# Kernel optimization log

Measured on AMD Instinct MI355X. Metric: run time of the kernel, lower is better.

The kernel has to match this reference:

```python
import jax, jax.numpy as jnp
import numpy as np
import math

B, T, D, H = 16, 256, 1024, 1024
SEG = 16              # segment_len
S = T // SEG          # number of cached segment slots (max_cached_segments=None)
SCALE = 1.0 / math.sqrt(H)


def _ln(x, g, b, eps=1e-5):
    m = jnp.mean(x, -1, keepdims=True)
    v = jnp.mean((x - m) ** 2, -1, keepdims=True)
    return (x - m) * jax.lax.rsqrt(v + eps) * g + b


def _lstm_cell(inp, h, c, Wih, Whh, bih, bhh):
    z = inp @ Wih.T + bih + h @ Whh.T + bhh
    i, f, g, o = jnp.split(z, 4, axis=-1)  # torch LSTMCell gate order i,f,g,o
    c2 = jax.nn.sigmoid(f) * c + jax.nn.sigmoid(i) * jnp.tanh(g)
    return jax.nn.sigmoid(o) * jnp.tanh(c2), c2


def setup_inputs() -> dict:
    key = jax.random.key(0)
    it = iter(jax.random.split(key, 40))

    def un(shape, fan):
        lim = 1.0 / np.sqrt(fan)
        return jax.random.uniform(next(it), shape, jnp.float32, -lim, lim)

    inp = {}
    inp['x'] = jax.random.normal(next(it), (B, T, D), jnp.float32)
    inp['W_ip'] = un((D, D), D); inp['b_ip'] = un((D,), D)
    inp['g_ip'] = jnp.ones((D,), jnp.float32); inp['be_ip'] = jnp.zeros((D,), jnp.float32)
    inp['W_ih0'] = un((4 * H, D), H); inp['W_hh0'] = un((4 * H, H), H)
    inp['b_ih0'] = un((4 * H,), H); inp['b_hh0'] = un((4 * H,), H)
    inp['W_ih1'] = un((4 * H, H), H); inp['W_hh1'] = un((4 * H, H), H)
    inp['b_ih1'] = un((4 * H,), H); inp['b_hh1'] = un((4 * H,), H)
    inp['Wq'] = un((H, H), H); inp['Wk'] = un((H, H), H); inp['Wv'] = un((H, H), H)
    inp['Wg1'] = un((H, 3 * H), 3 * H); inp['bg1'] = un((H,), 3 * H)
    inp['Wg2'] = un((H, H), H); inp['bg2'] = un((H,), H)
    inp['Wo'] = un((H, H), H); inp['bo'] = un((H,), H)
    inp['Wf'] = un((H, 2 * H), 2 * H); inp['bf'] = un((H,), 2 * H)
    inp['g_f'] = jnp.ones((H,), jnp.float32); inp['be_f'] = jnp.zeros((H,), jnp.float32)
    return inp


def reference(x, W_ip, b_ip, g_ip, be_ip,
              W_ih0, W_hh0, b_ih0, b_hh0,
              W_ih1, W_hh1, b_ih1, b_hh1,
              Wq, Wk, Wv, Wg1, bg1, Wg2, bg2, Wo, bo,
              Wf, bf, g_f, be_f):
    # input_proj (eval mode: dropout = identity)
    xp = jax.nn.relu(_ln(x @ W_ip.T + b_ip, g_ip, be_ip))      # [B,T,D]
    xseg = xp.transpose(1, 0, 2).reshape(S, SEG, B, D)          # [S,SEG,B,D]

    def seg_body(carry, xs):
        h0, c0, h1, c1, kbank, vbank = carry
        x_s, s = xs                                             # x_s:[SEG,B,D], s = #cached segments
        valid = jnp.arange(S) < s

        def step(inner, xt):
            h0, c0, h1, c1, seg_sum = inner
            h0, c0 = _lstm_cell(xt, h0, c0, W_ih0, W_hh0, b_ih0, b_hh0)
            h1, c1 = _lstm_cell(h0, h1, c1, W_ih1, W_hh1, b_ih1, b_hh1)
            # SegmentMemoryRetriever, cache_mode='gated_residual'
            q = h1 @ Wq.T
            scores = jnp.einsum('bh,sbh->bs', q, kbank) * SCALE
            scores = jnp.where(valid[None, :], scores, -1e9)
            attn = jax.nn.softmax(scores, axis=-1)
            retrieved = jnp.einsum('bs,sbh->bh', attn, vbank)
            gi = jnp.concatenate([h1, retrieved, h1 - retrieved], -1)
            gate = jax.nn.sigmoid(jax.nn.relu(gi @ Wg1.T + bg1) @ Wg2.T + bg2)
            out = (gate * h1 + (1.0 - gate) * retrieved) @ Wo.T + bo
            ret = jnp.where(s > 0, out, jnp.zeros_like(out))    # empty cache -> zero retrieval
            enh = jax.nn.relu(_ln(jnp.concatenate([h1, ret], -1) @ Wf.T + bf, g_f, be_f))
            return (h0, c0, h1, c1, seg_sum + h1), enh

        init = (h0, c0, h1, c1, jnp.zeros_like(h1))
        (h0, c0, h1, c1, seg_sum), enh = jax.lax.scan(step, init, x_s)
        # append segment to cache; keys/values projected once (linear, equivalent)
        kbank = kbank.at[s].set((seg_sum / SEG) @ Wk.T)         # context = segment mean (use_segment_context)
        vbank = vbank.at[s].set(h1 @ Wv.T)                      # memory = last top hidden of segment
        return (h0, c0, h1, c1, kbank, vbank), enh

    z = jnp.zeros((B, H), x.dtype)
    bank = jnp.zeros((S, B, H), x.dtype)
    carry0 = (z, z, z, z, bank, bank)
    _, enh = jax.lax.scan(seg_body, carry0, (xseg, jnp.arange(S)))
    return enh.reshape(T, B, H).transpose(1, 0, 2)              # sequence_output [B,T,H]
```

## Files before the change

kernel.cpp:

```cpp
#include <hip/hip_runtime.h>
#include <hip/hip_bf16.h>
#include <math.h>

#define B_ 16
#define T_ 256
#define D_ 1024
#define H_ 1024
#define S_ 16
#define SCALE_ (1.0f/32.0f)

typedef __attribute__((ext_vector_type(8))) short short8v;
typedef __attribute__((ext_vector_type(4))) float f32x4;

__device__ __forceinline__ float sigm(float x) { return 1.f / (1.f + expf(-x)); }

__device__ __forceinline__ ushort f2b(float v) {
  __hip_bfloat16 h = __float2bfloat16(v);
  return *reinterpret_cast<ushort*>(&h);
}
__device__ __forceinline__ float b2f(ushort u) {
  union { unsigned u32; float f; } x; x.u32 = ((unsigned)u) << 16; return x.f;
}

__device__ __forceinline__ void glds16(const void* g, void* l) {
  __builtin_amdgcn_global_load_lds((const __attribute__((address_space(1))) void*)g,
                                   (__attribute__((address_space(3))) void*)l, 16, 0, 0);
}

__device__ __forceinline__ void waitflags64(const int* f, int lane) {
  for (;;) {
    int v = __hip_atomic_load(f + lane, __ATOMIC_RELAXED, __HIP_MEMORY_SCOPE_AGENT);
    if (__all(v != 0)) return;
    __builtin_amdgcn_s_sleep(1);
  }
}

__device__ __forceinline__ void publish_pair(ushort* base, int tid, ushort hb) {
  unsigned hi = (unsigned)__shfl_down((int)hb, 1);
  if (!(tid & 1)) {
    unsigned word = (unsigned)hb | (hi << 16);
    __hip_atomic_exchange((unsigned*)base, word,
                          __ATOMIC_RELAXED, __HIP_MEMORY_SCOPE_AGENT);
  }
}

__device__ __forceinline__ float block_sum256(float v) {
  __shared__ float lds[4];
  #pragma unroll
  for (int off = 32; off; off >>= 1) v += __shfl_down(v, off);
  int w = threadIdx.x >> 6;
  if ((threadIdx.x & 63) == 0) lds[w] = v;
  __syncthreads();
  float r = lds[0] + lds[1] + lds[2] + lds[3];
  __syncthreads();
  return r;
}

#define NJOBS 14
struct CvtJobs {
  const float* src[NJOBS];
  ushort* dst[NJOBS];
  int cum[NJOBS + 1];
};

__global__ __launch_bounds__(256)
void cvt_all(CvtJobs J)
{
  int i = blockIdx.x * 256 + threadIdx.x;
  if (i >= J.cum[NJOBS]) return;
  int j = 0;
  #pragma unroll
  for (int k = 1; k < NJOBS; ++k) j += (i >= J.cum[k]) ? 1 : 0;
  int idx = i - J.cum[j];
  float4 v = ((const float4*)J.src[j])[idx];
  ushort4 o; o.x = f2b(v.x); o.y = f2b(v.y); o.z = f2b(v.z); o.w = f2b(v.w);
  ((ushort4*)J.dst[j])[idx] = o;
}

__global__ __launch_bounds__(256)
void cvt_bf16(const float* __restrict__ in, ushort* __restrict__ out, int n)
{
  int i = (blockIdx.x * 256 + threadIdx.x) * 4;
  if (i >= n) return;
  float4 v = *(const float4*)(in + i);
  ushort4 o; o.x = f2b(v.x); o.y = f2b(v.y); o.z = f2b(v.z); o.w = f2b(v.w);
  *(ushort4*)(out + i) = o;
}

template<int ACT, int REMAP>
__global__ __launch_bounds__(256)
void gemm_bf16(const ushort* __restrict__ A, const ushort* __restrict__ W,
               const float* __restrict__ bias,
               float* __restrict__ Cf, ushort* __restrict__ Cb,
               int M, int N, int K, float ascale, int ldc,
               const ushort* __restrict__ Hx, const float* __restrict__ Rx)
{
  __shared__ char As[16384];
  __shared__ char Bs[16384];
  const int tid = threadIdx.x;
  const int w = tid >> 6, l = tid & 63;
  const int m0 = blockIdx.y * 128, n0 = blockIdx.x * 128;
  const int wm = w >> 1, wn = w & 1;
  const int srow = l >> 3;
  const int sbyte = ((l & 7) * 16) ^ (srow << 4);
  f32x4 acc[4][4];
  #pragma unroll
  for (int i = 0; i < 4; ++i)
    #pragma unroll
    for (int j = 0; j < 4; ++j) acc[i][j] = (f32x4){0.f, 0.f, 0.f, 0.f};

  for (int k0 = 0; k0 < K; k0 += 64) {
    __syncthreads();
    #pragma unroll
    for (int c = 0; c < 4; ++c) {
      int ca = w * 4 + c;
      int r = ca * 8 + srow;
      glds16((const char*)A + (((size_t)(m0 + r) * K + k0) << 1) + sbyte, As + ca * 1024);
      glds16((const char*)W + (((size_t)(n0 + r) * K + k0) << 1) + sbyte, Bs + ca * 1024);
    }
    __syncthreads();
    #pragma unroll
    for (int ks = 0; ks < 2; ++ks) {
      short8v a[4], b[4];
      int qb = ks * 64 + (l >> 4) * 16;
      #pragma unroll
      for (int i = 0; i < 4; ++i) {
        int ra = wm * 64 + i * 16 + (l & 15);
        a[i] = *(const short8v*)(As + ra * 128 + (qb ^ ((ra & 7) << 4)));
        int rb = wn * 64 + i * 16 + (l & 15);
        b[i] = *(const short8v*)(Bs + rb * 128 + (qb ^ ((rb & 7) << 4)));
      }
      #pragma unroll
      for (int i = 0; i < 4; ++i)
        #pragma unroll
        for (int j = 0; j < 4; ++j)
          acc[i][j] = __builtin_amdgcn_mfma_f32_16x16x32_bf16(a[i], b[j], acc[i][j], 0, 0, 0);
    }
  }
  #pragma unroll
  for (int i = 0; i < 4; ++i) {
    #pragma unroll
    for (int j = 0; j < 4; ++j) {
      int n = n0 + wn * 64 + j * 16 + (l & 15);
      float bv = bias ? bias[n] : 0.f;
      #pragma unroll
      for (int q = 0; q < 4; ++q) {
        int m = m0 + wm * 64 + i * 16 + (l >> 4) * 4 + q;
        float v = acc[i][j][q] * ascale + bv;
        if (ACT == 1) v = fmaxf(v, 0.f);
        if (ACT == 2) v = sigm(v);
        if (ACT == 3) {
          float gte = sigm(v);
          float h = b2f(Hx[(size_t)m * 1024 + n]);
          float r = Rx[(size_t)m * 1024 + n];
          v = gte * h + (1.f - gte) * r;
        }
        if (ACT == 4) v = (m >= 256) ? v : 0.f;
        size_t off = REMAP ? ((size_t)((m & 255) * 16 + (m >> 8)) * ldc + n)
                           : ((size_t)m * ldc + n);
        if (Cf) Cf[off] = v;
        if (Cb) Cb[off] = f2b(v);
      }
    }
  }
}

__global__ __launch_bounds__(256)
void ln_relu_bf16(const float* __restrict__ X, const float* __restrict__ g,
                  const float* __restrict__ be, ushort* __restrict__ out)
{
  size_t row = blockIdx.x;
  const float4* p = (const float4*)(X + row * 1024);
  int tid = threadIdx.x;
  float4 v = p[tid];
  float s = block_sum256(v.x + v.y + v.z + v.w);
  float mean = s * (1.f / 1024.f);
  float dx = v.x - mean, dy = v.y - mean, dz = v.z - mean, dw = v.w - mean;
  float ss = block_sum256(dx*dx + dy*dy + dz*dz + dw*dw);
  float r = rsqrtf(ss * (1.f / 1024.f) + 1e-5f);
  int c4 = tid * 4;
  ushort4 o;
  o.x = f2b(fmaxf(dx * r * g[c4+0] + be[c4+0], 0.f));
  o.y = f2b(fmaxf(dy * r * g[c4+1] + be[c4+1], 0.f));
  o.z = f2b(fmaxf(dz * r * g[c4+2] + be[c4+2], 0.f));
  o.w = f2b(fmaxf(dw * r * g[c4+3] + be[c4+3], 0.f));
  *(ushort4*)(out + row * 1024 + c4) = o;
}

__global__ __launch_bounds__(256)
void ln_relu_final(const float* __restrict__ F, const float* __restrict__ g,
                   const float* __restrict__ be, float* __restrict__ out)
{
  int row = blockIdx.x;
  int t = row >> 4, b = row & 15;
  const float4* p = (const float4*)(F + (size_t)row * 1024);
  int tid = threadIdx.x;
  float4 v = p[tid];
  float s = block_sum256(v.x + v.y + v.z + v.w);
  float mean = s * (1.f / 1024.f);
  float dx = v.x - mean, dy = v.y - mean, dz = v.z - mean, dw = v.w - mean;
  float ss = block_sum256(dx*dx + dy*dy + dz*dz + dw*dw);
  float r = rsqrtf(ss * (1.f / 1024.f) + 1e-5f);
  int c4 = tid * 4;
  float4 o;
  o.x = fmaxf(dx * r * g[c4+0] + be[c4+0], 0.f);
  o.y = fmaxf(dy * r * g[c4+1] + be[c4+1], 0.f);
  o.z = fmaxf(dz * r * g[c4+2] + be[c4+2], 0.f);
  o.w = fmaxf(dw * r * g[c4+3] + be[c4+3], 0.f);
  ((float4*)(out + ((size_t)b * T_ + t) * 1024))[tid] = o;
}

__global__ __launch_bounds__(512)
void lstm_persistent(const ushort* __restrict__ Z0T,
                     const ushort* __restrict__ whh0,
                     const float* __restrict__ bhh0,
                     const ushort* __restrict__ wih1,
                     const ushort* __restrict__ whh1,
                     const float* __restrict__ bih1,
                     const float* __restrict__ bhh1,
                     ushort* __restrict__ HP,
                     ushort* __restrict__ H1B,
                     const ushort* __restrict__ ZP,
                     float* __restrict__ KSUM,
                     int* flag0,
                     int* flag1)
{
  __shared__ char Ah[65536];
  __shared__ float zs[8][16][16];
  __builtin_amdgcn_fence(__ATOMIC_ACQUIRE, "agent");
  const int tid = threadIdx.x, w = tid >> 6, l = tid & 63;
  const int lm = l & 15, lq = l >> 4;
  const int g = w & 3, kh = w >> 2;
  const int jb = blockIdx.x & 63;
  const int j0 = jb * 16;
  const int eb = tid >> 4, ej = tid & 15, jf = j0 + ej;
  float creg = 0.f;
  float br[4];

  if (blockIdx.x < 64) {
    short8v wreg[16];
    {
      const int n = g * 1024 + j0 + lm;
      const ushort* wb = whh0 + (size_t)n * 1024 + kh * 512 + lq * 8;
      #pragma unroll
      for (int ks = 0; ks < 16; ++ks) wreg[ks] = *(const short8v*)(wb + ks * 32);
    }
    if (tid < 256) {
      #pragma unroll
      for (int gg = 0; gg < 4; ++gg) br[gg] = bhh0[gg * 1024 + jf];
    }
    for (int t = 0; t < T_; ++t) {
      float z0v[4];
      if (tid < 256) {
        const ushort* zp = Z0T + ((size_t)t * 16 + eb) * 4096 + jf;
        #pragma unroll
        for (int gg = 0; gg < 4; ++gg) z0v[gg] = b2f(zp[gg * 1024]);
      }
      if (t > 0) {
        if (w == 0) waitflags64(flag0 + (size_t)t * 64, l);
        __syncthreads();
      }
      const ushort* hin = HP + (size_t)t * 16384;
      #pragma unroll
      for (int it = 0; it < 4; ++it) {
        int g1k = w * 4 + it;
        int kc = g1k * 4 + lq;
        int m = lm ^ (kc & 15);
        glds16(hin + (size_t)m * 1024 + kc * 8, Ah + g1k * 1024);
      }
      __syncthreads();
      {
        f32x4 a0 = {0.f,0.f,0.f,0.f}, a1 = {0.f,0.f,0.f,0.f};
        #pragma unroll
        for (int ks = 0; ks < 16; ks += 2) {
          int kc0 = kh * 64 + ks * 4 + lq;
          int kc1 = kc0 + 4;
          short8v f0 = *(const short8v*)(Ah + kc0 * 256 + ((lm ^ (kc0 & 15)) << 4));
          short8v f1 = *(const short8v*)(Ah + kc1 * 256 + ((lm ^ (kc1 & 15)) << 4));
          a0 = __builtin_amdgcn_mfma_f32_16x16x32_bf16(f0, wreg[ks],     a0, 0, 0, 0);
          a1 = __builtin_amdgcn_mfma_f32_16x16x32_bf16(f1, wreg[ks + 1], a1, 0, 0, 0);
        }
        #pragma unroll
        for (int q = 0; q < 4; ++q) zs[w][lq * 4 + q][lm] = a0[q] + a1[q];
      }
      __syncthreads();
      if (tid < 256) {
        float zi = zs[0][eb][ej] + zs[4][eb][ej] + z0v[0] + br[0];
        float zf = zs[1][eb][ej] + zs[5][eb][ej] + z0v[1] + br[1];
        float zg = zs[2][eb][ej] + zs[6][eb][ej] + z0v[2] + br[2];
        float zo = zs[3][eb][ej] + zs[7][eb][ej] + z0v[3] + br[3];
        float cp = sigm(zf) * creg + sigm(zi) * tanhf(zg);
        creg = cp;
        ushort hb = f2b(sigm(zo) * tanhf(cp));
        publish_pair(HP + (size_t)(t + 1) * 16384 + eb * 1024 + jf, tid, hb);
      }
      __syncthreads();
      if (tid == 0)
        __hip_atomic_store(flag0 + (size_t)(t + 1) * 64 + jb, 1,
                           __ATOMIC_RELAXED, __HIP_MEMORY_SCOPE_AGENT);
    }
  } else {
    short8v wreg[32];
    {
      const int n = g * 1024 + j0 + lm;
      const ushort* wb = (kh ? whh1 : wih1) + (size_t)n * 1024 + lq * 8;
      #pragma unroll
      for (int ks = 0; ks < 32; ++ks) wreg[ks] = *(const short8v*)(wb + ks * 32);
    }
    if (tid < 256) {
      #pragma unroll
      for (int gg = 0; gg < 4; ++gg)
        br[gg] = bih1[gg * 1024 + jf] + bhh1[gg * 1024 + jf];
    }
    float ksr = 0.f;
    for (int t = 0; t < T_; ++t) {
      if (w == 0) waitflags64(flag0 + (size_t)(t + 1) * 64, l);
      __syncthreads();
      const ushort* h0n = HP + (size_t)(t + 1) * 16384;
      #pragma unroll
      for (int it = 0; it < 4; ++it) {
        int g1k = w * 4 + it;
        int kc = g1k * 4 + lq;
        int m = lm ^ (kc & 15);
        glds16(h0n + (size_t)m * 1024 + kc * 8, Ah + g1k * 1024);
      }
      if (w == 1 && t > 0) waitflags64(flag1 + (size_t)(t - 1) * 64, l);
      __syncthreads();
      const ushort* h1p = (t > 0) ? (H1B + (size_t)(t - 1) * 16384) : ZP;
      #pragma unroll
      for (int it = 0; it < 4; ++it) {
        int g1k = 32 + w * 4 + it;
        int kc = g1k * 4 + lq;
        int m = lm ^ (kc & 15);
        glds16(h1p + (size_t)m * 1024 + (kc - 128) * 8, Ah + g1k * 1024);
      }
      __syncthreads();
      {
        f32x4 a0 = {0.f,0.f,0.f,0.f}, a1 = {0.f,0.f,0.f,0.f};
        #pragma unroll
        for (int ks = 0; ks < 32; ks += 2) {
          int kc0 = kh * 128 + ks * 4 + lq;
          int kc1 = kc0 + 4;
          short8v f0 = *(const short8v*)(Ah + kc0 * 256 + ((lm ^ (kc0 & 15)) << 4));
          short8v f1 = *(const short8v*)(Ah + kc1 * 256 + ((lm ^ (kc1 & 15)) << 4));
          a0 = __builtin_amdgcn_mfma_f32_16x16x32_bf16(f0, wreg[ks],     a0, 0, 0, 0);
          a1 = __builtin_amdgcn_mfma_f32_16x16x32_bf16(f1, wreg[ks + 1], a1, 0, 0, 0);
        }
        #pragma unroll
        for (int q = 0; q < 4; ++q) zs[w][lq * 4 + q][lm] = a0[q] + a1[q];
      }
      __syncthreads();
      if (tid < 256) {
        float zi = zs[0][eb][ej] + zs[4][eb][ej] + br[0];
        float zf = zs[1][eb][ej] + zs[5][eb][ej] + br[1];
        float zg = zs[2][eb][ej] + zs[6][eb][ej] + br[2];
        float zo = zs[3][eb][ej] + zs[7][eb][ej] + br[3];
        float cp = sigm(zf) * creg + sigm(zi) * tanhf(zg);
        creg = cp;
        float hv = sigm(zo) * tanhf(cp);
        ksr += hv;
        publish_pair(H1B + (size_t)t * 16384 + eb * 1024 + jf, tid, f2b(hv));
        if ((t & 15) == 15) {
          KSUM[((size_t)(t >> 4) * 16 + eb) * 1024 + jf] = ksr;
          ksr = 0.f;
        }
      }
      __syncthreads();
      if (tid == 0)
        __hip_atomic_store(flag1 + (size_t)t * 64 + jb, 1,
                           __ATOMIC_RELAXED, __HIP_MEMORY_SCOPE_AGENT);
    }
  }
}

__global__ __launch_bounds__(256)
void vgather(const ushort* __restrict__ H1B, ushort* __restrict__ VINB)
{
  int i = blockIdx.x * 256 + threadIdx.x;
  int row = i >> 8, c4 = (i & 255) * 4;
  int src = (row >> 4) * 256 + 240 + (row & 15);
  *(ushort4*)(VINB + (size_t)row * 1024 + c4) =
      *(const ushort4*)(H1B + (size_t)src * 1024 + c4);
}

__global__ __launch_bounds__(256)
void attn_kernel(const float* __restrict__ Q, const float* __restrict__ kbank,
                 const float* __restrict__ vbank, float* __restrict__ R)
{
  int row = blockIdx.x;
  int t = row >> 4, b = row & 15;
  int si = t >> 4;
  int tid = threadIdx.x, lane = tid & 63, w = tid >> 6;
  if (si == 0) {
    float4 z = {0.f, 0.f, 0.f, 0.f};
    ((float4*)(R + (size_t)row * 1024))[tid] = z;
    return;
  }
  __shared__ float sc[16];
  const float* q = Q + (size_t)row * 1024;
  for (int s = w; s < si; s += 4) {
    const float* kk = kbank + ((size_t)s * 16 + b) * 1024;
    float p = 0.f;
    for (int k = lane; k < 1024; k += 64) p += q[k] * kk[k];
    #pragma unroll
    for (int off = 32; off; off >>= 1) p += __shfl_down(p, off);
    if (lane == 0) sc[s] = p * SCALE_;
  }
  __syncthreads();
  float mx = -1e30f;
  for (int s = 0; s < si; ++s) mx = fmaxf(mx, sc[s]);
  float den = 0.f;
  for (int s = 0; s < si; ++s) den += expf(sc[s] - mx);
  float inv = 1.f / den;
  float4 accv = {0.f, 0.f, 0.f, 0.f};
  for (int s = 0; s < si; ++s) {
    float a = expf(sc[s] - mx) * inv;
    float4 vv = ((const float4*)(vbank + ((size_t)s * 16 + b) * 1024))[tid];
    accv.x += a * vv.x; accv.y += a * vv.y; accv.z += a * vv.z; accv.w += a * vv.w;
  }
  ((float4*)(R + (size_t)row * 1024))[tid] = accv;
}

__global__ __launch_bounds__(256)
void build_gi_cat(const ushort* __restrict__ H1B, const float* __restrict__ R,
                  ushort* __restrict__ GI, ushort* __restrict__ CATB)
{
  size_t r = blockIdx.x;
  int c4 = threadIdx.x * 4;
  ushort4 h4 = *(const ushort4*)(H1B + r * 1024 + c4);
  float4 rv = *(const float4*)(R + r * 1024 + c4);
  *(ushort4*)(GI + r * 3072 + c4) = h4;
  ushort4 rb; rb.x = f2b(rv.x); rb.y = f2b(rv.y); rb.z = f2b(rv.z); rb.w = f2b(rv.w);
  *(ushort4*)(GI + r * 3072 + 1024 + c4) = rb;
  ushort4 d;
  d.x = f2b(b2f(h4.x) - rv.x); d.y = f2b(b2f(h4.y) - rv.y);
  d.z = f2b(b2f(h4.z) - rv.z); d.w = f2b(b2f(h4.w) - rv.w);
  *(ushort4*)(GI + r * 3072 + 2048 + c4) = d;
  *(ushort4*)(CATB + r * 2048 + c4) = h4;
}

extern "C" void kernel_launch(void* const* d_in, const int* in_sizes, int n_in,
                              void* d_out, int out_size, void* d_ws, size_t ws_size,
                              hipStream_t stream) {
  const float* x     = (const float*)d_in[0];
  const float* W_ip  = (const float*)d_in[1];
  const float* b_ip  = (const float*)d_in[2];
  const float* g_ip  = (const float*)d_in[3];
  const float* be_ip = (const float*)d_in[4];
  const float* W_ih0 = (const float*)d_in[5];
  const float* W_hh0 = (const float*)d_in[6];
  const float* b_ih0 = (const float*)d_in[7];
  const float* b_hh0 = (const float*)d_in[8];
  const float* W_ih1 = (const float*)d_in[9];
  const float* W_hh1 = (const float*)d_in[10];
  const float* b_ih1 = (const float*)d_in[11];
  const float* b_hh1 = (const float*)d_in[12];
  const float* Wq    = (const float*)d_in[13];
  const float* Wk    = (const float*)d_in[14];
  const float* Wv    = (const float*)d_in[15];
  const float* Wg1   = (const float*)d_in[16];
  const float* bg1   = (const float*)d_in[17];
  const float* Wg2   = (const float*)d_in[18];
  const float* bg2   = (const float*)d_in[19];
  const float* Wo    = (const float*)d_in[20];
  const float* bo    = (const float*)d_in[21];
  const float* Wf    = (const float*)d_in[22];
  const float* bff   = (const float*)d_in[23];
  const float* g_f   = (const float*)d_in[24];
  const float* be_f  = (const float*)d_in[25];
  float* out = (float*)d_out;
  char* ws = (char*)d_ws;
  const size_t MB = (size_t)1 << 20;
  const size_t KB = (size_t)1 << 10;

  ushort* WB = (ushort*)(ws);
  ushort* wipB  = WB;
  ushort* wih0B = WB + 1*1048576;
  ushort* whh0B = WB + 5*1048576;
  ushort* wih1B = WB + 9*1048576;
  ushort* whh1B = WB + 13*1048576;
  ushort* wqB   = WB + 17*1048576;
  ushort* wkB   = WB + 18*1048576;
  ushort* wvB   = WB + 19*1048576;
  ushort* wg1B  = WB + 20*1048576;
  ushort* wg2B  = WB + 23*1048576;
  ushort* woB   = WB + 24*1048576;
  ushort* wfB   = WB + 25*1048576;

  ushort* XB   = (ushort*)(ws + 54 * MB);
  float*  XP   = (float*)(ws + 62 * MB);
  float*  Qf   = XP;
  char*   SCR  = ws + 78 * MB;
  ushort* Z0T  = (ushort*)SCR;
  ushort* GIB  = (ushort*)SCR;
  ushort* CATB = (ushort*)(SCR + 24 * MB);
  ushort* G1B  = (ushort*)(SCR + 40 * MB);
  ushort* MIXB = (ushort*)SCR;
  float*  FB   = (float*)SCR;
  ushort* H1B  = (ushort*)(ws + 126 * MB);
  ushort* HP   = (ushort*)(ws + 134 * MB);
  float*  R    = (float*)(ws + 134 * MB);
  char*   ST   = ws + 150 * MB;
  int*    flag0 = (int*)(ST);
  int*    flag1 = (int*)(ST + 68 * KB);
  const ushort* ZPc = (const ushort*)(ST + 132 * KB);
  float*  KSUM = (float*)(ST + 192 * KB);
  ushort* KSB  = (ushort*)(ST + 1216 * KB);
  float*  KBf  = (float*)(ST + 1728 * KB);
  float*  VBf  = (float*)(ST + 2752 * KB);
  ushort* VINB = (ushort*)(ST + 3776 * KB);

  hipMemsetAsync(ST, 0, 164 * KB, stream);
  hipMemsetAsync(HP, 0, 32 * KB, stream);

  dim3 blk(256);
  {
    CvtJobs J;
    const float* srcs[NJOBS] = { x, W_ip, W_ih0, W_hh0, W_ih1, W_hh1,
                                 Wq, Wk, Wv, Wg1, Wg2, Wo, Wf, nullptr };
    ushort* dsts[NJOBS] = { XB, wipB, wih0B, whh0B, wih1B, whh1B,
                            wqB, wkB, wvB, wg1B, wg2B, woB, wfB, nullptr };
    int n4[NJOBS] = { 1048576, 262144, 1048576, 1048576, 1048576, 1048576,
                      262144, 262144, 262144, 786432, 262144, 262144,
                      524288, 0 };
    int c = 0;
    for (int j = 0; j < NJOBS; ++j) {
      J.src[j] = srcs[j] ? srcs[j] : x;
      J.dst[j] = dsts[j] ? dsts[j] : XB;
      J.cum[j] = c;
      c += n4[j];
    }
    J.cum[NJOBS] = c;
    cvt_all<<<dim3((c + 255) / 256), blk, 0, stream>>>(J);
  }

  gemm_bf16<0,0><<<dim3(1024/128, 4096/128), blk, 0, stream>>>(
      XB, wipB, b_ip, XP, nullptr, 4096, 1024, 1024, 1.f, 1024, nullptr, nullptr);
  ln_relu_bf16<<<4096, blk, 0, stream>>>(XP, g_ip, be_ip, XB);
  gemm_bf16<0,1><<<dim3(4096/128, 4096/128), blk, 0, stream>>>(
      XB, wih0B, b_ih0, nullptr, Z0T, 4096, 4096, 1024, 1.f, 4096, nullptr, nullptr);
  {
    void* kargs[] = {
      (void*)&Z0T, (void*)&whh0B, (void*)&b_hh0,
      (void*)&wih1B, (void*)&whh1B, (void*)&b_ih1, (void*)&b_hh1,
      (void*)&HP, (void*)&H1B, (void*)&ZPc, (void*)&KSUM,
      (void*)&flag0, (void*)&flag1
    };
    hipLaunchCooperativeKernel((const void*)lstm_persistent,
                               dim3(128), dim3(512), kargs, 0, stream);
  }
  cvt_bf16<<<dim3(262144/4/256), blk, 0, stream>>>(KSUM, KSB, 262144);
  gemm_bf16<0,0><<<dim3(1024/128, 256/128), blk, 0, stream>>>(
      KSB, wkB, nullptr, KBf, nullptr, 256, 1024, 1024, 1.f/16.f, 1024, nullptr, nullptr);
  vgather<<<256, blk, 0, stream>>>(H1B, VINB);
  gemm_bf16<0,0><<<dim3(1024/128, 256/128), blk, 0, stream>>>(
      VINB, wvB, nullptr, VBf, nullptr, 256, 1024, 1024, 1.f, 1024, nullptr, nullptr);
  gemm_bf16<0,0><<<dim3(1024/128, 4096/128), blk, 0, stream>>>(
      H1B, wqB, nullptr, Qf, nullptr, 4096, 1024, 1024, 1.f, 1024, nullptr, nullptr);
  attn_kernel<<<4096, blk, 0, stream>>>(Qf, KBf, VBf, R);
  build_gi_cat<<<4096, blk, 0, stream>>>(H1B, R, GIB, CATB);
  gemm_bf16<1,0><<<dim3(1024/128, 4096/128), blk, 0, stream>>>(
      GIB, wg1B, bg1, nullptr, G1B, 4096, 1024, 3072, 1.f, 1024, nullptr, nullptr);
  gemm_bf16<3,0><<<dim3(1024/128, 4096/128), blk, 0, stream>>>(
      G1B, wg2B, bg2, nullptr, MIXB, 4096, 1024, 1024, 1.f, 1024, H1B, R);
  gemm_bf16<4,0><<<dim3(1024/128, 4096/128), blk, 0, stream>>>(
      MIXB, woB, bo, nullptr, CATB + 1024, 4096, 1024, 1024, 1.f, 2048, nullptr, nullptr);
  gemm_bf16<0,0><<<dim3(1024/128, 4096/128), blk, 0, stream>>>(
      CATB, wfB, bff, FB, nullptr, 4096, 1024, 2048, 1.f, 1024, nullptr, nullptr);
  ln_relu_final<<<4096, blk, 0, stream>>>(FB, g_f, be_f, out);
}
```

Baseline: 1.413 ms.

## Merge K/V bank GEMMs, fuse attention with gate-input build, store Q/K/V in bf16

Combines the KSUM conversion and the value-row gather into one prep kernel. The key and value projections become a single grouped GEMM that picks its weight and scale per M-block. Q, K and V are now written as bf16 instead of fp32, and the attention kernel also builds the gate-input and concat buffers directly. This removes several small launches and some fp32 round trips, but adds extra bf16 rounding in the attention scores and values.

```diff
diff --git a/kernel.cpp b/kernel.cpp
--- a/kernel.cpp
+++ b/kernel.cpp
@@ -77,29 +77,22 @@
   ((ushort4*)J.dst[j])[idx] = o;
 }
 
-__global__ __launch_bounds__(256)
-void cvt_bf16(const float* __restrict__ in, ushort* __restrict__ out, int n)
-{
-  int i = (blockIdx.x * 256 + threadIdx.x) * 4;
-  if (i >= n) return;
-  float4 v = *(const float4*)(in + i);
-  ushort4 o; o.x = f2b(v.x); o.y = f2b(v.y); o.z = f2b(v.z); o.w = f2b(v.w);
-  *(ushort4*)(out + i) = o;
-}
-
 template<int ACT, int REMAP>
 __global__ __launch_bounds__(256)
 void gemm_bf16(const ushort* __restrict__ A, const ushort* __restrict__ W,
                const float* __restrict__ bias,
                float* __restrict__ Cf, ushort* __restrict__ Cb,
                int M, int N, int K, float ascale, int ldc,
-               const ushort* __restrict__ Hx, const float* __restrict__ Rx)
+               const ushort* __restrict__ Hx, const float* __restrict__ Rx,
+               const ushort* __restrict__ W2, float ascale2, int msplit)
 {
   __shared__ char As[16384];
   __shared__ char Bs[16384];
   const int tid = threadIdx.x;
   const int w = tid >> 6, l = tid & 63;
   const int m0 = blockIdx.y * 128, n0 = blockIdx.x * 128;
+  const ushort* __restrict__ Wp = (m0 < msplit) ? W : W2;
+  const float asc = (m0 < msplit) ? ascale : ascale2;
   const int wm = w >> 1, wn = w & 1;
   const int srow = l >> 3;
   const int sbyte = ((l & 7) * 16) ^ (srow << 4);
@@ -116,7 +109,7 @@
       int ca = w * 4 + c;
       int r = ca * 8 + srow;
       glds16((const char*)A + (((size_t)(m0 + r) * K + k0) << 1) + sbyte, As + ca * 1024);
-      glds16((const char*)W + (((size_t)(n0 + r) * K + k0) << 1) + sbyte, Bs + ca * 1024);
+      glds16((const char*)Wp + (((size_t)(n0 + r) * K + k0) << 1) + sbyte, Bs + ca * 1024);
     }
     __syncthreads();
     #pragma unroll
@@ -146,7 +139,7 @@
       #pragma unroll
       for (int q = 0; q < 4; ++q) {
         int m = m0 + wm * 64 + i * 16 + (l >> 4) * 4 + q;
-        float v = acc[i][j][q] * ascale + bv;
+        float v = acc[i][j][q] * asc + bv;
         if (ACT == 1) v = fmaxf(v, 0.f);
         if (ACT == 2) v = sigm(v);
         if (ACT == 3) {
@@ -374,67 +367,65 @@
 }
 
 __global__ __launch_bounds__(256)
-void vgather(const ushort* __restrict__ H1B, ushort* __restrict__ VINB)
-{
-  int i = blockIdx.x * 256 + threadIdx.x;
-  int row = i >> 8, c4 = (i & 255) * 4;
-  int src = (row >> 4) * 256 + 240 + (row & 15);
-  *(ushort4*)(VINB + (size_t)row * 1024 + c4) =
+void prep_banks(const float* __restrict__ KSUM, ushort* __restrict__ KSB,
+                const ushort* __restrict__ H1B)
+{
+  int r = blockIdx.x;
+  int c4 = threadIdx.x * 4;
+  float4 v = *(const float4*)(KSUM + (size_t)r * 1024 + c4);
+  ushort4 o; o.x = f2b(v.x); o.y = f2b(v.y); o.z = f2b(v.z); o.w = f2b(v.w);
+  *(ushort4*)(KSB + (size_t)r * 1024 + c4) = o;
+  int src = (r >> 4) * 256 + 240 + (r & 15);
+  *(ushort4*)(KSB + (size_t)(256 + r) * 1024 + c4) =
       *(const ushort4*)(H1B + (size_t)src * 1024 + c4);
 }
 
 __global__ __launch_bounds__(256)
-void attn_kernel(const float* __restrict__ Q, const float* __restrict__ kbank,
-                 const float* __restrict__ vbank, float* __restrict__ R)
+void attn_gi_cat(const ushort* __restrict__ Q, const ushort* __restrict__ kbank,
+                 const ushort* __restrict__ vbank, const ushort* __restrict__ H1B,
+                 float* __restrict__ R, ushort* __restrict__ GI,
+                 ushort* __restrict__ CATB)
 {
   int row = blockIdx.x;
   int t = row >> 4, b = row & 15;
   int si = t >> 4;
   int tid = threadIdx.x, lane = tid & 63, w = tid >> 6;
-  if (si == 0) {
-    float4 z = {0.f, 0.f, 0.f, 0.f};
-    ((float4*)(R + (size_t)row * 1024))[tid] = z;
-    return;
-  }
   __shared__ float sc[16];
-  const float* q = Q + (size_t)row * 1024;
-  for (int s = w; s < si; s += 4) {
-    const float* kk = kbank + ((size_t)s * 16 + b) * 1024;
-    float p = 0.f;
-    for (int k = lane; k < 1024; k += 64) p += q[k] * kk[k];
-    #pragma unroll
-    for (int off = 32; off; off >>= 1) p += __shfl_down(p, off);
-    if (lane == 0) sc[s] = p * SCALE_;
-  }
-  __syncthreads();
-  float mx = -1e30f;
-  for (int s = 0; s < si; ++s) mx = fmaxf(mx, sc[s]);
-  float den = 0.f;
-  for (int s = 0; s < si; ++s) den += expf(sc[s] - mx);
-  float inv = 1.f / den;
   float4 accv = {0.f, 0.f, 0.f, 0.f};
-  for (int s = 0; s < si; ++s) {
-    float a = expf(sc[s] - mx) * inv;
-    float4 vv = ((const float4*)(vbank + ((size_t)s * 16 + b) * 1024))[tid];
-    accv.x += a * vv.x; accv.y += a * vv.y; accv.z += a * vv.z; accv.w += a * vv.w;
-  }
-  ((float4*)(R + (size_t)row * 1024))[tid] = accv;
-}
-
-__global__ __launch_bounds__(256)
-void build_gi_cat(const ushort* __restrict__ H1B, const float* __restrict__ R,
-                  ushort* __restrict__ GI, ushort* __restrict__ CATB)
-{
-  size_t r = blockIdx.x;
-  int c4 = threadIdx.x * 4;
+  if (si > 0) {
+    const ushort* q = Q + (size_t)row * 1024;
+    for (int s = w; s < si; s += 4) {
+      const ushort* kk = kbank + ((size_t)s * 16 + b) * 1024;
+      float p = 0.f;
+      for (int k = lane; k < 1024; k += 64) p += b2f(q[k]) * b2f(kk[k]);
+      #pragma unroll
+      for (int off = 32; off; off >>= 1) p += __shfl_down(p, off);
+      if (lane == 0) sc[s] = p * SCALE_;
+    }
+    __syncthreads();
+    float mx = -1e30f;
+    for (int s = 0; s < si; ++s) mx = fmaxf(mx, sc[s]);
+    float den = 0.f;
+    for (int s = 0; s < si; ++s) den += expf(sc[s] - mx);
+    float inv = 1.f / den;
+    for (int s = 0; s < si; ++s) {
+      float a = expf(sc[s] - mx) * inv;
+      ushort4 vv = *(const ushort4*)(vbank + ((size_t)s * 16 + b) * 1024 + tid * 4);
+      accv.x += a * b2f(vv.x); accv.y += a * b2f(vv.y);
+      accv.z += a * b2f(vv.z); accv.w += a * b2f(vv.w);
+    }
+  }
+  size_t r = row;
+  int c4 = tid * 4;
+  ((float4*)(R + r * 1024))[tid] = accv;
   ushort4 h4 = *(const ushort4*)(H1B + r * 1024 + c4);
-  float4 rv = *(const float4*)(R + r * 1024 + c4);
   *(ushort4*)(GI + r * 3072 + c4) = h4;
-  ushort4 rb; rb.x = f2b(rv.x); rb.y = f2b(rv.y); rb.z = f2b(rv.z); rb.w = f2b(rv.w);
+  ushort4 rb; rb.x = f2b(accv.x); rb.y = f2b(accv.y);
+  rb.z = f2b(accv.z); rb.w = f2b(accv.w);
   *(ushort4*)(GI + r * 3072 + 1024 + c4) = rb;
   ushort4 d;
-  d.x = f2b(b2f(h4.x) - rv.x); d.y = f2b(b2f(h4.y) - rv.y);
-  d.z = f2b(b2f(h4.z) - rv.z); d.w = f2b(b2f(h4.w) - rv.w);
+  d.x = f2b(b2f(h4.x) - accv.x); d.y = f2b(b2f(h4.y) - accv.y);
+  d.z = f2b(b2f(h4.z) - accv.z); d.w = f2b(b2f(h4.w) - accv.w);
   *(ushort4*)(GI + r * 3072 + 2048 + c4) = d;
   *(ushort4*)(CATB + r * 2048 + c4) = h4;
 }
@@ -489,7 +480,7 @@
 
   ushort* XB   = (ushort*)(ws + 54 * MB);
   float*  XP   = (float*)(ws + 62 * MB);
-  float*  Qf   = XP;
+  ushort* QB   = (ushort*)(ws + 62 * MB);
   char*   SCR  = ws + 78 * MB;
   ushort* Z0T  = (ushort*)SCR;
   ushort* GIB  = (ushort*)SCR;
@@ -506,9 +497,8 @@
   const ushort* ZPc = (const ushort*)(ST + 132 * KB);
   float*  KSUM = (float*)(ST + 192 * KB);
   ushort* KSB  = (ushort*)(ST + 1216 * KB);
-  float*  KBf  = (float*)(ST + 1728 * KB);
-  float*  VBf  = (float*)(ST + 2752 * KB);
-  ushort* VINB = (ushort*)(ST + 3776 * KB);
+  ushort* KBb  = (ushort*)(ST + 2240 * KB);
+  ushort* VBb  = KBb + 256 * 1024;
 
   hipMemsetAsync(ST, 0, 164 * KB, stream);
   hipMemsetAsync(HP, 0, 32 * KB, stream);
@@ -534,11 +524,14 @@
     cvt_all<<<dim3((c + 255) / 256), blk, 0, stream>>>(J);
   }
 
+  const int BIG = 1 << 30;
   gemm_bf16<0,0><<<dim3(1024/128, 4096/128), blk, 0, stream>>>(
-      XB, wipB, b_ip, XP, nullptr, 4096, 1024, 1024, 1.f, 1024, nullptr, nullptr);
+      XB, wipB, b_ip, XP, nullptr, 4096, 1024, 1024, 1.f, 1024,
+      nullptr, nullptr, wipB, 1.f, BIG);
   ln_relu_bf16<<<4096, blk, 0, stream>>>(XP, g_ip, be_ip, XB);
   gemm_bf16<0,1><<<dim3(4096/128, 4096/128), blk, 0, stream>>>(
-      XB, wih0B, b_ih0, nullptr, Z0T, 4096, 4096, 1024, 1.f, 4096, nullptr, nullptr);
+      XB, wih0B, b_ih0, nullptr, Z0T, 4096, 4096, 1024, 1.f, 4096,
+      nullptr, nullptr, wih0B, 1.f, BIG);
   {
     void* kargs[] = {
       (void*)&Z0T, (void*)&whh0B, (void*)&b_hh0,
@@ -549,23 +542,25 @@
     hipLaunchCooperativeKernel((const void*)lstm_persistent,
                                dim3(128), dim3(512), kargs, 0, stream);
   }
-  cvt_bf16<<<dim3(262144/4/256), blk, 0, stream>>>(KSUM, KSB, 262144);
-  gemm_bf16<0,0><<<dim3(1024/128, 256/128), blk, 0, stream>>>(
-      KSB, wkB, nullptr, KBf, nullptr, 256, 1024, 1024, 1.f/16.f, 1024, nullptr, nullptr);
-  vgather<<<256, blk, 0, stream>>>(H1B, VINB);
-  gemm_bf16<0,0><<<dim3(1024/128, 256/128), blk, 0, stream>>>(
-      VINB, wvB, nullptr, VBf, nullptr, 256, 1024, 1024, 1.f, 1024, nullptr, nullptr);
+  prep_banks<<<256, blk, 0, stream>>>(KSUM, KSB, H1B);
+  gemm_bf16<0,0><<<dim3(1024/128, 512/128), blk, 0, stream>>>(
+      KSB, wkB, nullptr, nullptr, KBb, 512, 1024, 1024, 1.f/16.f, 1024,
+      nullptr, nullptr, wvB, 1.f, 256);
   gemm_bf16<0,0><<<dim3(1024/128, 4096/128), blk, 0, stream>>>(
-      H1B, wqB, nullptr, Qf, nullptr, 4096, 1024, 1024, 1.f, 1024, nullptr, nullptr);
-  attn_kernel<<<4096, blk, 0, stream>>>(Qf, KBf, VBf, R);
-  build_gi_cat<<<4096, blk, 0, stream>>>(H1B, R, GIB, CATB);
+      H1B, wqB, nullptr, nullptr, QB, 4096, 1024, 1024, 1.f, 1024,
+      nullptr, nullptr, wqB, 1.f, BIG);
+  attn_gi_cat<<<4096, blk, 0, stream>>>(QB, KBb, VBb, H1B, R, GIB, CATB);
   gemm_bf16<1,0><<<dim3(1024/128, 4096/128), blk, 0, stream>>>(
-      GIB, wg1B, bg1, nullptr, G1B, 4096, 1024, 3072, 1.f, 1024, nullptr, nullptr);
+      GIB, wg1B, bg1, nullptr, G1B, 4096, 1024, 3072, 1.f, 1024,
+      nullptr, nullptr, wg1B, 1.f, BIG);
   gemm_bf16<3,0><<<dim3(1024/128, 4096/128), blk, 0, stream>>>(
-      G1B, wg2B, bg2, nullptr, MIXB, 4096, 1024, 1024, 1.f, 1024, H1B, R);
+      G1B, wg2B, bg2, nullptr, MIXB, 4096, 1024, 1024, 1.f, 1024,
+      H1B, R, wg2B, 1.f, BIG);
   gemm_bf16<4,0><<<dim3(1024/128, 4096/128), blk, 0, stream>>>(
-      MIXB, woB, bo, nullptr, CATB + 1024, 4096, 1024, 1024, 1.f, 2048, nullptr, nullptr);
+      MIXB, woB, bo, nullptr, CATB + 1024, 4096, 1024, 1024, 1.f, 2048,
+      nullptr, nullptr, woB, 1.f, BIG);
   gemm_bf16<0,0><<<dim3(1024/128, 4096/128), blk, 0, stream>>>(
-      CATB, wfB, bff, FB, nullptr, 4096, 1024, 2048, 1.f, 1024, nullptr, nullptr);
+      CATB, wfB, bff, FB, nullptr, 4096, 1024, 2048, 1.f, 1024,
+      nullptr, nullptr, wfB, 1.f, BIG);
   ln_relu_final<<<4096, blk, 0, stream>>>(FB, g_f, be_f, out);
 }
```

Result: faster. 1.378 ms (-2.5%).
